# Optimization experiments

Hardware: AMD Instinct MI355X
Metric: run time of the kernel (lower is better)

## Reference

```python
import jax, jax.numpy as jnp
import numpy as np

N_HEADS, IN_F, COND_IN, OUT_F = 8, 16, 32, 32
B = 32768


def setup_inputs() -> dict:
    key = jax.random.key(0)
    k1, k2, k3, k4 = jax.random.split(key, 4)
    return {
        "input": jax.random.normal(k1, (N_HEADS, B, IN_F), dtype=jnp.float32),
        "cond": jax.random.normal(k2, (N_HEADS, B, COND_IN), dtype=jnp.float32),
        "cond_weight": jax.random.normal(k3, (N_HEADS, OUT_F * (IN_F + 1), COND_IN), dtype=jnp.float32) * 0.1,
        "cond_bias": jax.random.normal(k4, (N_HEADS, OUT_F * (IN_F + 1)), dtype=jnp.float32) * 0.1,
    }


def reference(input, cond, cond_weight, cond_bias):
    h, b, in_f = input.shape
    out_f = cond_weight.shape[1] // (in_f + 1)
    # hypernetwork: generate per-sample weights (h, b, out*(in+1))
    w = jnp.einsum('hbc,hkc->hbk', cond, cond_weight) + cond_bias[:, None, :]
    w = w.reshape(h, b, out_f, in_f + 1)  # (h, b, out, in+1)
    # append homogeneous 1 for bias column, then per-sample matvec
    x1 = jnp.concatenate([input, jnp.ones((h, b, 1), dtype=input.dtype)], axis=-1)
    return jnp.einsum('hboi,hbi->hbo', w, x1)
```

## Files before the change

### kernel.cpp

```cpp
#include <hip/hip_runtime.h>

#define NH    8
#define BROWS 32768
#define INF   16
#define CIN   32
#define OUTF  32
#define KTOT  544

#define XBLK   96
#define PAIRS  (XBLK * 2)
#define TPAIRS (BROWS / 32)

typedef __attribute__((ext_vector_type(8))) short short8;
typedef __attribute__((ext_vector_type(4))) float floatx4;

__device__ __forceinline__ short f2bf(float f) {
    __bf16 h = (__bf16)f;
    return __builtin_bit_cast(short, h);
}

__global__ __launch_bounds__(256, 3) void meta_multilinear(
    const float* __restrict__ input,
    const float* __restrict__ cond,
    const float* __restrict__ weight,
    const float* __restrict__ bias,
    float* __restrict__ out)
{
    const int tid   = threadIdx.x;
    const int lane  = tid & 63;
    const int wave  = tid >> 6;
    const int pair  = wave >> 1;
    const int otile = wave & 1;
    const int r     = lane & 15;
    const int quad  = lane >> 4;
    const int c0    = quad * 8;

    const int h = blockIdx.y;
    const int o = otile * 16 + r;

    const float* Wh = weight + (size_t)h * KTOT * CIN;
    const float* bh = bias   + (size_t)h * KTOT;

    short8 wfrag[17];
    #pragma unroll
    for (int i = 0; i < 17; ++i) {
        const float* src = Wh + (o * 17 + i) * CIN + c0;
        floatx4 w0 = *(const floatx4*)(src);
        floatx4 w1 = *(const floatx4*)(src + 4);
        short8 f;
        f[0]=f2bf(w0.x); f[1]=f2bf(w0.y); f[2]=f2bf(w0.z); f[3]=f2bf(w0.w);
        f[4]=f2bf(w1.x); f[5]=f2bf(w1.y); f[6]=f2bf(w1.z); f[7]=f2bf(w1.w);
        wfrag[i] = f;
    }

    short8 bA;
    #pragma unroll
    for (int j = 0; j < 8; ++j) {
        const int i = c0 + j;
        short v = 0;
        if (i < 17) v = f2bf(bh[o * 17 + i]);
        bA[j] = v;
    }

    const int pairId = blockIdx.x * 2 + pair;

    const float* condh = cond  + (size_t)h * BROWS * CIN;
    const float* inh   = input + (size_t)h * BROWS * INF;
    float*       outh  = out   + (size_t)h * BROWS * OUTF;
    const floatx4 zero = {0.f, 0.f, 0.f, 0.f};

    #define COMPUTE_TILE(cA, cB, x0, x1, x2, x3, brow) do {                          \
        short8 cf;                                                                   \
        cf[0]=f2bf(cA.x); cf[1]=f2bf(cA.y); cf[2]=f2bf(cA.z); cf[3]=f2bf(cA.w);      \
        cf[4]=f2bf(cB.x); cf[5]=f2bf(cB.y); cf[6]=f2bf(cB.z); cf[7]=f2bf(cB.w);      \
        short8 xb;                                                                   \
        if (quad == 0) {                                                             \
            xb[0]=f2bf(x0.x); xb[1]=f2bf(x0.y); xb[2]=f2bf(x0.z); xb[3]=f2bf(x0.w);  \
            xb[4]=f2bf(x1.x); xb[5]=f2bf(x1.y); xb[6]=f2bf(x1.z); xb[7]=f2bf(x1.w);  \
        } else if (quad == 1) {                                                      \
            xb[0]=f2bf(x2.x); xb[1]=f2bf(x2.y); xb[2]=f2bf(x2.z); xb[3]=f2bf(x2.w);  \
            xb[4]=f2bf(x3.x); xb[5]=f2bf(x3.y); xb[6]=f2bf(x3.z); xb[7]=f2bf(x3.w);  \
        } else if (quad == 2) {                                                      \
            xb[0]=f2bf(1.0f); xb[1]=0; xb[2]=0; xb[3]=0;                             \
            xb[4]=0; xb[5]=0; xb[6]=0; xb[7]=0;                                      \
        } else {                                                                     \
            xb[0]=0; xb[1]=0; xb[2]=0; xb[3]=0;                                      \
            xb[4]=0; xb[5]=0; xb[6]=0; xb[7]=0;                                      \
        }                                                                            \
        floatx4 f0 = __builtin_amdgcn_mfma_f32_16x16x32_bf16(bA, xb, zero, 0, 0, 0); \
        floatx4 f1 = zero;                                                           \
        STEP(0,  x0.x); STEP(1,  x0.y); STEP(2,  x0.z); STEP(3,  x0.w);              \
        STEP(4,  x1.x); STEP(5,  x1.y); STEP(6,  x1.z); STEP(7,  x1.w);              \
        STEP(8,  x2.x); STEP(9,  x2.y); STEP(10, x2.z); STEP(11, x2.w);              \
        STEP(12, x3.x); STEP(13, x3.y); STEP(14, x3.z); STEP(15, x3.w);              \
        STEP(16, 1.0f);                                                              \
        const floatx4 facc = f0 + f1;                                                \
        float* dst = outh + (size_t)((brow) + r) * OUTF + otile * 16 + quad * 4;     \
        __builtin_nontemporal_store(facc, (floatx4*)dst);                            \
    } while (0)

    #define STEP(i, s) do {                                                          \
        floatx4 d_ = __builtin_amdgcn_mfma_f32_16x16x32_bf16(wfrag[(i)], cf, zero, 0, 0, 0); \
        if ((i) & 1) f1 += d_ * (s); else f0 += d_ * (s);                            \
    } while (0)

    for (int tp = pairId; tp < TPAIRS; tp += PAIRS) {
        const int bA0 = tp * 32;
        const int bB0 = bA0 + 16;

        const float* crowA = condh + (size_t)(bA0 + r) * CIN + c0;
        floatx4 cAa = *(const floatx4*)(crowA);
        floatx4 cBa = *(const floatx4*)(crowA + 4);
        const float* xrowA = inh + (size_t)(bA0 + r) * INF;
        floatx4 x0a = *(const floatx4*)(xrowA);
        floatx4 x1a = *(const floatx4*)(xrowA + 4);
        floatx4 x2a = *(const floatx4*)(xrowA + 8);
        floatx4 x3a = *(const floatx4*)(xrowA + 12);

        const float* crowB = condh + (size_t)(bB0 + r) * CIN + c0;
        floatx4 cAb = *(const floatx4*)(crowB);
        floatx4 cBb = *(const floatx4*)(crowB + 4);
        const float* xrowB = inh + (size_t)(bB0 + r) * INF;
        floatx4 x0b = *(const floatx4*)(xrowB);
        floatx4 x1b = *(const floatx4*)(xrowB + 4);
        floatx4 x2b = *(const floatx4*)(xrowB + 8);
        floatx4 x3b = *(const floatx4*)(xrowB + 12);

        COMPUTE_TILE(cAa, cBa, x0a, x1a, x2a, x3a, bA0);
        COMPUTE_TILE(cAb, cBb, x0b, x1b, x2b, x3b, bB0);
    }

    #undef STEP
    #undef COMPUTE_TILE
}

extern "C" void kernel_launch(void* const* d_in, const int* in_sizes, int n_in,
                              void* d_out, int out_size, void* d_ws, size_t ws_size,
                              hipStream_t stream) {
    const float* input  = (const float*)d_in[0];
    const float* cond   = (const float*)d_in[1];
    const float* weight = (const float*)d_in[2];
    const float* bias   = (const float*)d_in[3];
    float* out = (float*)d_out;

    dim3 grid(XBLK, NH, 1);
    dim3 block(256, 1, 1);
    hipLaunchKernelGGL(meta_multilinear, grid, block, 0, stream,
                       input, cond, weight, bias, out);
}
```

Baseline: 122.8 us.

## Stage weight fragments in LDS and give each wave both output tiles

Weight fragments are converted to bf16 once per block and kept in shared memory instead of 17 register fragments per wave. Each wave now computes both 16-wide output tiles for its 32 rows. Previously the two output tiles were split across two waves, and each of those waves loaded and converted the same cond/input rows. Removing that duplicate global loading and conversion, together with the lower register pressure, allows occupancy to rise to 4 blocks per SIMD and a larger grid. The cost is an LDS read per MFMA step and a block-wide barrier after the weight staging.

Result: slower. 169.6 us (+38.1%).

```diff
diff --git a/kernel.cpp b/kernel.cpp
--- a/kernel.cpp
+++ b/kernel.cpp
@@ -7,9 +7,9 @@
 #define OUTF  32
 #define KTOT  544
 
-#define XBLK   96
-#define PAIRS  (XBLK * 2)
-#define TPAIRS (BROWS / 32)
+#define BLKX  128
+#define WPH   (BLKX * 4)
+#define UNITS (BROWS / 32)
 
 typedef __attribute__((ext_vector_type(8))) short short8;
 typedef __attribute__((ext_vector_type(4))) float floatx4;
@@ -19,119 +19,145 @@
     return __builtin_bit_cast(short, h);
 }
 
-__global__ __launch_bounds__(256, 3) void meta_multilinear(
+__global__ __launch_bounds__(256, 4) void meta_multilinear(
     const float* __restrict__ input,
     const float* __restrict__ cond,
     const float* __restrict__ weight,
     const float* __restrict__ bias,
     float* __restrict__ out)
 {
+    __shared__ short8 lds_w[17 * 2 * 64];
+
     const int tid   = threadIdx.x;
     const int lane  = tid & 63;
     const int wave  = tid >> 6;
-    const int pair  = wave >> 1;
-    const int otile = wave & 1;
     const int r     = lane & 15;
     const int quad  = lane >> 4;
     const int c0    = quad * 8;
 
     const int h = blockIdx.y;
-    const int o = otile * 16 + r;
 
     const float* Wh = weight + (size_t)h * KTOT * CIN;
     const float* bh = bias   + (size_t)h * KTOT;
 
-    short8 wfrag[17];
-    #pragma unroll
-    for (int i = 0; i < 17; ++i) {
-        const float* src = Wh + (o * 17 + i) * CIN + c0;
+    for (int s = tid; s < 17 * 2 * 64; s += 256) {
+        const int sl = s & 63;
+        const int sr = sl & 15;
+        const int sq = sl >> 4;
+        const int ot = (s >> 6) & 1;
+        const int i  = s >> 7;
+        const float* src = Wh + (size_t)((ot * 16 + sr) * 17 + i) * CIN + sq * 8;
         floatx4 w0 = *(const floatx4*)(src);
         floatx4 w1 = *(const floatx4*)(src + 4);
         short8 f;
         f[0]=f2bf(w0.x); f[1]=f2bf(w0.y); f[2]=f2bf(w0.z); f[3]=f2bf(w0.w);
         f[4]=f2bf(w1.x); f[5]=f2bf(w1.y); f[6]=f2bf(w1.z); f[7]=f2bf(w1.w);
-        wfrag[i] = f;
+        lds_w[s] = f;
     }
 
-    short8 bA;
+    short8 bA0, bA1;
     #pragma unroll
     for (int j = 0; j < 8; ++j) {
         const int i = c0 + j;
-        short v = 0;
-        if (i < 17) v = f2bf(bh[o * 17 + i]);
-        bA[j] = v;
+        short v0 = 0, v1 = 0;
+        if (i < 17) {
+            v0 = f2bf(bh[r * 17 + i]);
+            v1 = f2bf(bh[(16 + r) * 17 + i]);
+        }
+        bA0[j] = v0;
+        bA1[j] = v1;
     }
 
-    const int pairId = blockIdx.x * 2 + pair;
+    __syncthreads();
 
     const float* condh = cond  + (size_t)h * BROWS * CIN;
     const float* inh   = input + (size_t)h * BROWS * INF;
     float*       outh  = out   + (size_t)h * BROWS * OUTF;
     const floatx4 zero = {0.f, 0.f, 0.f, 0.f};
 
-    #define COMPUTE_TILE(cA, cB, x0, x1, x2, x3, brow) do {                          \
-        short8 cf;                                                                   \
-        cf[0]=f2bf(cA.x); cf[1]=f2bf(cA.y); cf[2]=f2bf(cA.z); cf[3]=f2bf(cA.w);      \
-        cf[4]=f2bf(cB.x); cf[5]=f2bf(cB.y); cf[6]=f2bf(cB.z); cf[7]=f2bf(cB.w);      \
-        short8 xb;                                                                   \
-        if (quad == 0) {                                                             \
-            xb[0]=f2bf(x0.x); xb[1]=f2bf(x0.y); xb[2]=f2bf(x0.z); xb[3]=f2bf(x0.w);  \
-            xb[4]=f2bf(x1.x); xb[5]=f2bf(x1.y); xb[6]=f2bf(x1.z); xb[7]=f2bf(x1.w);  \
-        } else if (quad == 1) {                                                      \
-            xb[0]=f2bf(x2.x); xb[1]=f2bf(x2.y); xb[2]=f2bf(x2.z); xb[3]=f2bf(x2.w);  \
-            xb[4]=f2bf(x3.x); xb[5]=f2bf(x3.y); xb[6]=f2bf(x3.z); xb[7]=f2bf(x3.w);  \
-        } else if (quad == 2) {                                                      \
-            xb[0]=f2bf(1.0f); xb[1]=0; xb[2]=0; xb[3]=0;                             \
-            xb[4]=0; xb[5]=0; xb[6]=0; xb[7]=0;                                      \
-        } else {                                                                     \
-            xb[0]=0; xb[1]=0; xb[2]=0; xb[3]=0;                                      \
-            xb[4]=0; xb[5]=0; xb[6]=0; xb[7]=0;                                      \
-        }                                                                            \
-        floatx4 f0 = __builtin_amdgcn_mfma_f32_16x16x32_bf16(bA, xb, zero, 0, 0, 0); \
-        floatx4 f1 = zero;                                                           \
-        STEP(0,  x0.x); STEP(1,  x0.y); STEP(2,  x0.z); STEP(3,  x0.w);              \
-        STEP(4,  x1.x); STEP(5,  x1.y); STEP(6,  x1.z); STEP(7,  x1.w);              \
-        STEP(8,  x2.x); STEP(9,  x2.y); STEP(10, x2.z); STEP(11, x2.w);              \
-        STEP(12, x3.x); STEP(13, x3.y); STEP(14, x3.z); STEP(15, x3.w);              \
-        STEP(16, 1.0f);                                                              \
-        const floatx4 facc = f0 + f1;                                                \
-        float* dst = outh + (size_t)((brow) + r) * OUTF + otile * 16 + quad * 4;     \
-        __builtin_nontemporal_store(facc, (floatx4*)dst);                            \
-    } while (0)
+    const int gw = blockIdx.x * 4 + wave;
 
-    #define STEP(i, s) do {                                                          \
-        floatx4 d_ = __builtin_amdgcn_mfma_f32_16x16x32_bf16(wfrag[(i)], cf, zero, 0, 0, 0); \
-        if ((i) & 1) f1 += d_ * (s); else f0 += d_ * (s);                            \
-    } while (0)
+    for (int u = gw; u < UNITS; u += WPH) {
+        const int ba = u * 32;
+        const int bb = ba + 16;
 
-    for (int tp = pairId; tp < TPAIRS; tp += PAIRS) {
-        const int bA0 = tp * 32;
-        const int bB0 = bA0 + 16;
-
-        const float* crowA = condh + (size_t)(bA0 + r) * CIN + c0;
+        const float* crowA = condh + (size_t)(ba + r) * CIN + c0;
         floatx4 cAa = *(const floatx4*)(crowA);
         floatx4 cBa = *(const floatx4*)(crowA + 4);
-        const float* xrowA = inh + (size_t)(bA0 + r) * INF;
+        const float* xrowA = inh + (size_t)(ba + r) * INF;
         floatx4 x0a = *(const floatx4*)(xrowA);
         floatx4 x1a = *(const floatx4*)(xrowA + 4);
         floatx4 x2a = *(const floatx4*)(xrowA + 8);
         floatx4 x3a = *(const floatx4*)(xrowA + 12);
 
-        const float* crowB = condh + (size_t)(bB0 + r) * CIN + c0;
+        const float* crowB = condh + (size_t)(bb + r) * CIN + c0;
         floatx4 cAb = *(const floatx4*)(crowB);
         floatx4 cBb = *(const floatx4*)(crowB + 4);
-        const float* xrowB = inh + (size_t)(bB0 + r) * INF;
+        const float* xrowB = inh + (size_t)(bb + r) * INF;
         floatx4 x0b = *(const floatx4*)(xrowB);
         floatx4 x1b = *(const floatx4*)(xrowB + 4);
         floatx4 x2b = *(const floatx4*)(xrowB + 8);
         floatx4 x3b = *(const floatx4*)(xrowB + 12);
 
-        COMPUTE_TILE(cAa, cBa, x0a, x1a, x2a, x3a, bA0);
-        COMPUTE_TILE(cAb, cBb, x0b, x1b, x2b, x3b, bB0);
+        short8 cfa, cfb;
+        cfa[0]=f2bf(cAa.x); cfa[1]=f2bf(cAa.y); cfa[2]=f2bf(cAa.z); cfa[3]=f2bf(cAa.w);
+        cfa[4]=f2bf(cBa.x); cfa[5]=f2bf(cBa.y); cfa[6]=f2bf(cBa.z); cfa[7]=f2bf(cBa.w);
+        cfb[0]=f2bf(cAb.x); cfb[1]=f2bf(cAb.y); cfb[2]=f2bf(cAb.z); cfb[3]=f2bf(cAb.w);
+        cfb[4]=f2bf(cBb.x); cfb[5]=f2bf(cBb.y); cfb[6]=f2bf(cBb.z); cfb[7]=f2bf(cBb.w);
+
+        #define MAKE_XB(xb, x0, x1, x2, x3) do {                                     \
+            if (quad == 0) {                                                         \
+                xb[0]=f2bf(x0.x); xb[1]=f2bf(x0.y); xb[2]=f2bf(x0.z); xb[3]=f2bf(x0.w); \
+                xb[4]=f2bf(x1.x); xb[5]=f2bf(x1.y); xb[6]=f2bf(x1.z); xb[7]=f2bf(x1.w); \
+            } else if (quad == 1) {                                                  \
+                xb[0]=f2bf(x2.x); xb[1]=f2bf(x2.y); xb[2]=f2bf(x2.z); xb[3]=f2bf(x2.w); \
+                xb[4]=f2bf(x3.x); xb[5]=f2bf(x3.y); xb[6]=f2bf(x3.z); xb[7]=f2bf(x3.w); \
+            } else if (quad == 2) {                                                  \
+                xb[0]=f2bf(1.0f); xb[1]=0; xb[2]=0; xb[3]=0;                         \
+                xb[4]=0; xb[5]=0; xb[6]=0; xb[7]=0;                                  \
+            } else {                                                                 \
+                xb[0]=0; xb[1]=0; xb[2]=0; xb[3]=0;                                  \
+                xb[4]=0; xb[5]=0; xb[6]=0; xb[7]=0;                                  \
+            }                                                                        \
+        } while (0)
+        short8 xba, xbb;
+        MAKE_XB(xba, x0a, x1a, x2a, x3a);
+        MAKE_XB(xbb, x0b, x1b, x2b, x3b);
+        #undef MAKE_XB
+
+        floatx4 fa0 = __builtin_amdgcn_mfma_f32_16x16x32_bf16(bA0, xba, zero, 0, 0, 0);
+        floatx4 fa1 = __builtin_amdgcn_mfma_f32_16x16x32_bf16(bA1, xba, zero, 0, 0, 0);
+        floatx4 fb0 = __builtin_amdgcn_mfma_f32_16x16x32_bf16(bA0, xbb, zero, 0, 0, 0);
+        floatx4 fb1 = __builtin_amdgcn_mfma_f32_16x16x32_bf16(bA1, xbb, zero, 0, 0, 0);
+
+        #define STEP(i, sa, sb) do {                                                 \
+            short8 w0 = lds_w[(i) * 128 + lane];                                     \
+            short8 w1 = lds_w[(i) * 128 + 64 + lane];                                \
+            floatx4 d00 = __builtin_amdgcn_mfma_f32_16x16x32_bf16(w0, cfa, zero, 0, 0, 0); \
+            floatx4 d01 = __builtin_amdgcn_mfma_f32_16x16x32_bf16(w1, cfa, zero, 0, 0, 0); \
+            floatx4 d10 = __builtin_amdgcn_mfma_f32_16x16x32_bf16(w0, cfb, zero, 0, 0, 0); \
+            floatx4 d11 = __builtin_amdgcn_mfma_f32_16x16x32_bf16(w1, cfb, zero, 0, 0, 0); \
+            fa0 += d00 * (sa); fa1 += d01 * (sa);                                    \
+            fb0 += d10 * (sb); fb1 += d11 * (sb);                                    \
+        } while (0)
+        STEP(0,  x0a.x, x0b.x); STEP(1,  x0a.y, x0b.y);
+        STEP(2,  x0a.z, x0b.z); STEP(3,  x0a.w, x0b.w);
+        STEP(4,  x1a.x, x1b.x); STEP(5,  x1a.y, x1b.y);
+        STEP(6,  x1a.z, x1b.z); STEP(7,  x1a.w, x1b.w);
+        STEP(8,  x2a.x, x2b.x); STEP(9,  x2a.y, x2b.y);
+        STEP(10, x2a.z, x2b.z); STEP(11, x2a.w, x2b.w);
+        STEP(12, x3a.x, x3b.x); STEP(13, x3a.y, x3b.y);
+        STEP(14, x3a.z, x3b.z); STEP(15, x3a.w, x3b.w);
+        STEP(16, 1.0f,  1.0f);
+        #undef STEP
+
+        float* da = outh + (size_t)(ba + r) * OUTF + quad * 4;
+        __builtin_nontemporal_store(fa0, (floatx4*)da);
+        __builtin_nontemporal_store(fa1, (floatx4*)(da + 16));
+        float* db = outh + (size_t)(bb + r) * OUTF + quad * 4;
+        __builtin_nontemporal_store(fb0, (floatx4*)db);
+        __builtin_nontemporal_store(fb1, (floatx4*)(db + 16));
     }
-
-    #undef STEP
-    #undef COMPUTE_TILE
 }
 
 extern "C" void kernel_launch(void* const* d_in, const int* in_sizes, int n_in,
@@ -143,7 +169,7 @@
     const float* bias   = (const float*)d_in[3];
     float* out = (float*)d_out;
 
-    dim3 grid(XBLK, NH, 1);
+    dim3 grid(BLKX, NH, 1);
     dim3 block(256, 1, 1);
     hipLaunchKernelGGL(meta_multilinear, grid, block, 0, stream,
                        input, cond, weight, bias, out);
```
